# Kernel tuning notes

Hardware: AMD Instinct MI355X
Metric: run time of the kernel (lower is better)

The kernel has to match this reference:

```python
import jax, jax.numpy as jnp
from jax import lax
import numpy as np

B, T, H, W = 32, 16, 64, 64
LAT, HID, NL = 256, 256, 10
CH = 32  # c_hid
DN = ('NCHW', 'OIHW', 'NCHW')


def setup_inputs() -> dict:
    key = jax.random.key(0)
    keys = iter(jax.random.split(key, 64))
    def rn(shape, scale=0.05):
        return jax.random.normal(next(keys), shape, jnp.float32) * scale
    inp = {}
    inp['x'] = jax.random.normal(next(keys), (B, T, H, W), jnp.float32)
    inp['t'] = jax.random.normal(next(keys), (B, T, H, W), jnp.float32)
    # encoder convs (torch Conv2d weight layout: (out,in,kh,kw))
    inp['ec1_w'] = rn((CH, 1, 3, 3));        inp['ec1_b'] = rn((CH,))
    inp['ec2_w'] = rn((CH, CH, 3, 3));       inp['ec2_b'] = rn((CH,))
    inp['ec3_w'] = rn((2*CH, CH, 3, 3));     inp['ec3_b'] = rn((2*CH,))
    inp['ec4_w'] = rn((2*CH, 2*CH, 3, 3));   inp['ec4_b'] = rn((2*CH,))
    inp['ec5_w'] = rn((2*CH, 2*CH, 3, 3));   inp['ec5_b'] = rn((2*CH,))
    inp['el_w'] = rn((LAT, 2*CH*8*8));       inp['el_b'] = rn((LAT,))
    # decoder (ConvTranspose2d weight layout: (in,out,kh,kw))
    inp['dl_w'] = rn((2*CH*8*8, LAT));       inp['dl_b'] = rn((2*CH*8*8,))
    inp['dt1_w'] = rn((2*CH, 2*CH, 3, 3));   inp['dt1_b'] = rn((2*CH,))
    inp['dc1_w'] = rn((2*CH, 2*CH, 3, 3));   inp['dc1_b'] = rn((2*CH,))
    inp['dt2_w'] = rn((2*CH, CH, 3, 3));     inp['dt2_b'] = rn((CH,))
    inp['dc2_w'] = rn((CH, CH, 3, 3));       inp['dc2_b'] = rn((CH,))
    inp['dt3_w'] = rn((CH, 1, 3, 3));        inp['dt3_b'] = rn((1,))
    # 10 stacked LSTMCells (LAT == HID so layer 0 weight shape matches the rest)
    inp['Wih'] = rn((NL, 4*HID, HID))
    inp['Whh'] = rn((NL, 4*HID, HID))
    inp['bih'] = rn((NL, 4*HID))
    inp['bhh'] = rn((NL, 4*HID))
    inp['lw'] = rn((LAT, HID));  inp['lb'] = rn((LAT,))
    return inp


def gelu(v):
    return jax.nn.gelu(v, approximate=False)


def conv(x, w, b, stride):
    y = lax.conv_general_dilated(x, w, (stride, stride), [(1, 1), (1, 1)], dimension_numbers=DN)
    return y + b[None, :, None, None]


def tconv(x, w, b):
    # torch ConvTranspose2d(k=3, stride=2, padding=1, output_padding=1):
    # flip kernel, swap in/out channels, lhs_dilation=2, pad (lo=1, hi=2)
    wf = jnp.transpose(w[:, :, ::-1, ::-1], (1, 0, 2, 3))
    y = lax.conv_general_dilated(x, wf, (1, 1), [(1, 2), (1, 2)], lhs_dilation=(2, 2), dimension_numbers=DN)
    return y + b[None, :, None, None]


def reference(x, t, ec1_w, ec1_b, ec2_w, ec2_b, ec3_w, ec3_b, ec4_w, ec4_b, ec5_w, ec5_b,
              el_w, el_b, dl_w, dl_b, dt1_w, dt1_b, dc1_w, dc1_b, dt2_w, dt2_b,
              dc2_w, dc2_b, dt3_w, dt3_b, Wih, Whh, bih, bhh, lw, lb):

    def encode(imgs):                              # (N,1,64,64) -> (N,LAT)
        h = gelu(conv(imgs, ec1_w, ec1_b, 2))      # 32x32
        h = gelu(conv(h, ec2_w, ec2_b, 1))
        h = gelu(conv(h, ec3_w, ec3_b, 2))         # 16x16
        h = gelu(conv(h, ec4_w, ec4_b, 1))
        h = gelu(conv(h, ec5_w, ec5_b, 2))         # 8x8
        return h.reshape(h.shape[0], -1) @ el_w.T + el_b

    def decode(z):                                 # (N,LAT) -> (N,1,64,64)
        h = gelu(z @ dl_w.T + dl_b).reshape(z.shape[0], 2*CH, 8, 8)
        h = gelu(tconv(h, dt1_w, dt1_b))           # 16x16
        h = gelu(conv(h, dc1_w, dc1_b, 1))
        h = gelu(tconv(h, dt2_w, dt2_b))           # 32x32
        h = gelu(conv(h, dc2_w, dc2_b, 1))
        return jnp.tanh(tconv(h, dt3_w, dt3_b))    # 64x64

    def cell_stack(h, c, xin):                     # h,c: (NL,B,HID)
        hs, cs = [], []
        prev = xin
        for l in range(NL):
            z = prev @ Wih[l].T + bih[l] + h[l] @ Whh[l].T + bhh[l]
            i, f, g, o = jnp.split(z, 4, axis=-1)
            cl = jax.nn.sigmoid(f) * c[l] + jax.nn.sigmoid(i) * jnp.tanh(g)
            hl = jax.nn.sigmoid(o) * jnp.tanh(cl)
            hs.append(hl); cs.append(cl); prev = hl
        out = prev @ lw.T + lb                     # skip=False
        return jnp.stack(hs), jnp.stack(cs), out

    f_x_t = jnp.concatenate((x, t), axis=1)        # (B,2T,H,W)
    z_x_t = encode(f_x_t.reshape(-1, 1, H, W)).reshape(B, 2 * T, LAT)
    z_x = z_x_t[:, :T]

    h0 = jnp.zeros((NL, B, HID), x.dtype)
    c0 = jnp.zeros((NL, B, HID), x.dtype)

    def step1(carry, xin):
        h, c = carry
        h, c, out = cell_stack(h, c, xin)
        return (h, c), out

    (hT, cT), outs1 = lax.scan(step1, (h0, c0), jnp.swapaxes(z_x, 0, 1))

    def step2(carry, _):
        h, c, xin = carry
        h, c, out = cell_stack(h, c, xin)
        return (h, c, out), out

    _, outs2 = lax.scan(step2, (hT, cT, outs1[-1]), None, length=T)

    outputs = jnp.swapaxes(jnp.concatenate((outs1, outs2), axis=0), 0, 1)  # (B,2T,LAT)
    y_t = outputs[:, T - 1:-1]                    # (B,T,LAT)

    f_t_ = decode(y_t.reshape(B * T, LAT))        # (B*T,1,H,W)
    loss_pred = jnp.mean((f_t_ - f_x_t[:, T:].reshape(-1, 1, H, W)) ** 2)

    f_x_ = decode(z_x.reshape(B * T, LAT))        # rec_loss=True branch
    loss_rec = jnp.mean((f_x_ - f_x_t[:, :T].reshape(-1, 1, H, W)) ** 2)

    return loss_pred, loss_rec, f_t_.reshape(B, T, H, W)
```

## Files before the change

### kernel.cpp

```cpp
#include <hip/hip_runtime.h>
#include <math.h>

#define DEV __device__ __forceinline__

typedef __attribute__((ext_vector_type(8))) short bf8_t;
typedef __attribute__((ext_vector_type(4))) float f4_t;
typedef unsigned short us;

DEV float sigm_f(float v) { return 1.0f / (1.0f + __expf(-v)); }
DEV float tanh_f(float v) { return fmaf(-2.0f, 1.0f / (1.0f + __expf(2.0f * v)), 1.0f); }
DEV float gelu_f(float v) {
  float u = 0.79788456080f * fmaf(0.044715f * v * v, v, v);
  return 0.5f * v * (1.0f + tanh_f(u));
}
DEV unsigned short f2bf(float f) {
  unsigned u = __float_as_uint(f);
  u = (u + 0x7FFFu + ((u >> 16) & 1u)) >> 16;
  return (unsigned short)u;
}
DEV void astore(unsigned* p, unsigned v) {
  __hip_atomic_store(p, v, __ATOMIC_RELAXED, __HIP_MEMORY_SCOPE_AGENT);
}

DEV void prep_norm(int li, const float* w, us* wb, int CIN) {
  int ci = li % CIN;
  int r  = li / CIN;
  int kw = r % 3; r /= 3;
  int kh = r % 3;
  int co = r / 3;
  wb[li] = f2bf(w[((co * CIN + ci) * 3 + kh) * 3 + kw]);
}
DEV void prep_par(int li, const float* w, us* wb, int COUT, int CIN) {
  const int TAPORD[9] = {4, 3, 5, 1, 7, 0, 2, 6, 8};
  int ci = li % CIN;
  int r  = li / CIN;
  int ti = r % 9;
  int co = r / 9;
  int tap = TAPORD[ti];
  int kh = tap / 3, kw = tap % 3;
  wb[li] = f2bf(w[((ci * COUT + co) * 3 + (2 - kh)) * 3 + (2 - kw)]);
}

__global__ __launch_bounds__(256) void prepw_all_k(
    const float* __restrict__ ec2, const float* __restrict__ ec3,
    const float* __restrict__ ec4, const float* __restrict__ ec5,
    const float* __restrict__ dt1, const float* __restrict__ dc1,
    const float* __restrict__ dt2, const float* __restrict__ dc2,
    us* __restrict__ o_ec2, us* __restrict__ o_ec3,
    us* __restrict__ o_ec4, us* __restrict__ o_ec5,
    us* __restrict__ o_dt1, us* __restrict__ o_dc1,
    us* __restrict__ o_dt2, us* __restrict__ o_dc2)
{
  int idx = blockIdx.x * 256 + threadIdx.x;
  if (idx < 9216)        prep_norm(idx,          ec2, o_ec2, 32);
  else if (idx < 27648)  prep_norm(idx - 9216,   ec3, o_ec3, 32);
  else if (idx < 64512)  prep_norm(idx - 27648,  ec4, o_ec4, 64);
  else if (idx < 101376) prep_norm(idx - 64512,  ec5, o_ec5, 64);
  else if (idx < 138240) prep_par (idx - 101376, dt1, o_dt1, 64, 64);
  else if (idx < 175104) prep_norm(idx - 138240, dc1, o_dc1, 64);
  else if (idx < 193536) prep_par (idx - 175104, dt2, o_dt2, 32, 64);
  else if (idx < 202752) prep_norm(idx - 193536, dc2, o_dc2, 32);
}

__global__ __launch_bounds__(256) void prep_misc_k(
    const float* __restrict__ Wih, const float* __restrict__ lw,
    const float* __restrict__ lb,  const float* __restrict__ bih,
    us* __restrict__ wih0b, us* __restrict__ lwTb,
    us* __restrict__ lwbp,  float* __restrict__ beff)
{
  int idx = blockIdx.x * 256 + threadIdx.x;
  if (idx < 262144) {
    wih0b[idx] = f2bf(Wih[idx]);
  } else if (idx < 327680) {
    int i = idx - 262144;
    int n = i & 255, kcol = i >> 8;
    lwTb[i] = f2bf(lw[(size_t)n * 256 + kcol]);
  } else if (idx < 393216) {
    int i = idx - 327680;
    lwbp[i] = f2bf(lw[i]);
  } else if (idx < 394240) {
    int j = idx - 393216;
    float s = bih[j];
    const float* row = Wih + (size_t)j * 256;
    for (int n = 0; n < 256; ++n) s = fmaf(row[n], lb[n], s);
    beff[j] = s;
  }
}

__global__ __launch_bounds__(256) void prep_eldl_k(
    const float* __restrict__ el_w, const float* __restrict__ dl_w,
    us* __restrict__ elWb, us* __restrict__ dlWb)
{
  int idx = blockIdx.x * 256 + threadIdx.x;
  if (idx < 1048576) {
    int i = idx;
    int kn = i & 4095, n = i >> 12;
    elWb[i] = f2bf(el_w[(size_t)n * 4096 + ((kn & 63) * 64 + (kn >> 6))]);
  } else {
    int i = idx - 1048576;
    int k = i & 255, nout = i >> 8;
    dlWb[i] = f2bf(dl_w[(size_t)((nout & 63) * 64 + (nout >> 6)) * 256 + k]);
  }
}

__global__ __launch_bounds__(256) void prep_wl1_k(
    const us* __restrict__ src, us* __restrict__ wb)
{
  int idx = blockIdx.x * 256 + threadIdx.x;
  int e = idx & 7, lane = (idx >> 3) & 63, ks = (idx >> 9) & 7, nt = idx >> 12;
  wb[idx] = src[(size_t)(nt * 16 + (lane & 15)) * 256 + ks * 32 + (lane >> 4) * 8 + e];
}

__global__ __launch_bounds__(256) void ec1_k(
    const float* __restrict__ x, const float* __restrict__ t,
    const float* __restrict__ w, const float* __restrict__ bias,
    us* __restrict__ out)
{
  __shared__ float sw[288];
  __shared__ float sb[32];
  for (int i = threadIdx.x; i < 288; i += 256) sw[i] = w[i];
  if (threadIdx.x < 32) sb[threadIdx.x] = bias[threadIdx.x];
  __syncthreads();
  int idx = blockIdx.x * 256 + threadIdx.x;
  int ox = idx & 31, oy = (idx >> 5) & 31, n = idx >> 10;
  int b = n >> 5, j = n & 31;
  const float* ip = (j < 16) ? (x + (size_t)(b * 16 + j) * 4096)
                             : (t + (size_t)(b * 16 + j - 16) * 4096);
  float pv[9];
#pragma unroll
  for (int kh = 0; kh < 3; ++kh) {
    int iy = oy * 2 + kh - 1;
#pragma unroll
    for (int kw = 0; kw < 3; ++kw) {
      int ix = ox * 2 + kw - 1;
      pv[kh * 3 + kw] = ((unsigned)iy < 64u && (unsigned)ix < 64u) ? ip[iy * 64 + ix] : 0.f;
    }
  }
  us u[32];
#pragma unroll
  for (int co = 0; co < 32; ++co) {
    float a = sb[co];
#pragma unroll
    for (int i = 0; i < 9; ++i) a = fmaf(pv[i], sw[co * 9 + i], a);
    u[co] = f2bf(gelu_f(a));
  }
  us* op = out + (size_t)idx * 32;
#pragma unroll
  for (int p = 0; p < 4; ++p) {
    uint4 v;
    v.x = u[p*8+0] | (u[p*8+1] << 16);
    v.y = u[p*8+2] | (u[p*8+3] << 16);
    v.z = u[p*8+4] | (u[p*8+5] << 16);
    v.w = u[p*8+6] | (u[p*8+7] << 16);
    *(uint4*)&op[p * 8] = v;
  }
}

template<int CIN, int COUT, int HIN, int WIN, int TH, int TW, int MODE>
DEV void convmf_tile(const us* __restrict__ in, const us* __restrict__ wb,
                     const float* __restrict__ bias, us* __restrict__ out,
                     int vb, int nofs, us* lds)
{
  constexpr int HO  = (MODE == 1) ? HIN / 2 : HIN;
  constexpr int WO  = (MODE == 1) ? WIN / 2 : WIN;
  constexpr int TIH = (MODE == 1) ? 2 * TH + 1 : TH + 2;
  constexpr int TIW = (MODE == 1) ? 2 * TW + 1 : TW + 2;
  constexpr int TIWP = (TIW & 1) ? TIW : TIW + 1;
  constexpr int CG  = CIN / 8;
  constexpr int K   = 9 * CIN;
  constexpr int KS  = K / 32;
  constexpr int NT  = COUT / 16;
  constexpr int MT  = (TH * TW) / 16;
  constexpr int MPW = MT / 4;
  constexpr int TY  = HO / TH, TX = WO / TW;

  const int n = nofs + vb / (TY * TX);
  const int trem = vb % (TY * TX);
  const int ty0 = (trem / TX) * TH, tx0 = (trem % TX) * TW;

  constexpr int ENT = TIH * TIW * CG;
  for (int e = threadIdx.x; e < ENT; e += 256) {
    int txx = e % TIW;
    int rr  = e / TIW;
    int cg  = rr % CG;
    int tyy = rr / CG;
    int iy, ix; bool ok;
    if (MODE == 0) {
      iy = ty0 + tyy - 1; ix = tx0 + txx - 1;
      ok = (unsigned)iy < (unsigned)HIN && (unsigned)ix < (unsigned)WIN;
    } else {
      iy = 2 * ty0 + tyy - 1; ix = 2 * tx0 + txx - 1;
      ok = (unsigned)iy < (unsigned)HIN && (unsigned)ix < (unsigned)WIN;
    }
    int4 val = {0, 0, 0, 0};
    if (ok) val = *(const int4*)&in[(((size_t)n * HIN + iy) * WIN + ix) * CIN + cg * 8];
    *(int4*)&lds[(size_t)((tyy * CG + cg) * TIWP + txx) * 8] = val;
  }
  __syncthreads();

  const int lane = threadIdx.x & 63, wv = threadIdx.x >> 6;
  const int l15 = lane & 15, l4 = lane >> 4;

  f4_t acc[MPW][NT] = {};
  for (int ks = 0; ks < KS; ++ks) {
    const int tap = (ks * 32) / CIN;
    const int kh = tap / 3, kw = tap % 3;
    const int cb = ((ks * 32) % CIN) / 8 + l4;
    bf8_t bf[NT];
#pragma unroll
    for (int nt = 0; nt < NT; ++nt)
      bf[nt] = *(const bf8_t*)&wb[(size_t)(nt * 16 + l15) * K + ks * 32 + 8 * l4];
#pragma unroll
    for (int mi = 0; mi < MPW; ++mi) {
      int m = (wv * MPW + mi) * 16 + l15;
      int oy = m / TW, ox = m % TW;
      int rt = ((MODE == 1) ? 2 * oy : oy) + kh;
      int ct = ((MODE == 1) ? 2 * ox : ox) + kw;
      bf8_t a = *(const bf8_t*)&lds[(size_t)((rt * CG + cb) * TIWP + ct) * 8];
#pragma unroll
      for (int nt = 0; nt < NT; ++nt)
        acc[mi][nt] = __builtin_amdgcn_mfma_f32_16x16x32_bf16(a, bf[nt], acc[mi][nt], 0, 0, 0);
    }
  }

#pragma unroll
  for (int mi = 0; mi < MPW; ++mi) {
    int mbase = (wv * MPW + mi) * 16;
#pragma unroll
    for (int nt = 0; nt < NT; ++nt) {
      int co = nt * 16 + l15;
      float bv = bias[co];
#pragma unroll
      for (int r = 0; r < 4; ++r) {
        int m = mbase + l4 * 4 + r;
        int oy = m / TW, ox = m % TW;
        float v = acc[mi][nt][r] + bv;
        out[(((size_t)n * HO + ty0 + oy) * WO + (tx0 + ox)) * COUT + co] = f2bf(gelu_f(v));
      }
    }
  }
  __syncthreads();
}

template<int CIN, int COUT, int HIN, int WIN, int TH, int TW, int MODE>
__global__ __launch_bounds__(256) void convmf_k(
    const us* __restrict__ in, const us* __restrict__ wb,
    const float* __restrict__ bias, us* __restrict__ out)
{
  constexpr int TIH = (MODE == 1) ? 2 * TH + 1 : TH + 2;
  constexpr int TIW = (MODE == 1) ? 2 * TW + 1 : TW + 2;
  constexpr int TIWP = (TIW & 1) ? TIW : TIW + 1;
  __shared__ us lds[TIH * TIWP * (CIN / 8) * 8];
  convmf_tile<CIN, COUT, HIN, WIN, TH, TW, MODE>(in, wb, bias, out, blockIdx.x, 0, lds);
}

template<int CIN, int COUT, int HIN, int WIN, int SH, int SW>
DEV void tconvp_tile(const us* __restrict__ in, const us* __restrict__ wbp,
                     const float* __restrict__ bias, us* __restrict__ out,
                     int vb, int nofs, us* lds)
{
  constexpr int HO = 2 * HIN, WO = 2 * WIN;
  constexpr int CG = CIN / 8;
  constexpr int TIH = SH + 1, TIW = SW + 1;
  constexpr int NT = COUT / 16;
  constexpr int MPW_P = (SH * SW) / 16;
  constexpr int TY = HIN / SH, TX = WIN / SW;

  const int n = nofs + vb / (TY * TX);
  const int trem = vb % (TY * TX);
  const int toy = trem / TX, tox = trem % TX;
  const int ty0s = toy * SH, tx0s = tox * SW;

  constexpr int ENT = TIH * TIW * CG;
  for (int e = threadIdx.x; e < ENT; e += 256) {
    int txx = e % TIW;
    int rr  = e / TIW;
    int cg  = rr % CG;
    int tyy = rr / CG;
    int iy = ty0s + tyy, ix = tx0s + txx;
    int4 val = {0, 0, 0, 0};
    if (iy < HIN && ix < WIN)
      val = *(const int4*)&in[(((size_t)n * HIN + iy) * WIN + ix) * CIN + cg * 8];
    *(int4*)&lds[(size_t)((tyy * CG + cg) * TIW + txx) * 8] = val;
  }
  __syncthreads();

  const int lane = threadIdx.x & 63, wv = threadIdx.x >> 6;
  const int l15 = lane & 15, l4 = lane >> 4;
  const int dy = wv >> 1, dx = wv & 1;
  const int NXT = 1 + dx;
  const int KS2 = ((1 + dy) * (1 + dx) * CIN) / 32;
  const int koff = (dy ? (dx ? 5 : 3) : (dx ? 1 : 0)) * CIN;

  f4_t acc[MPW_P][NT] = {};
  for (int ks = 0; ks < KS2; ++ks) {
    const int tapi = (ks * 32) / CIN;
    const int cb = ((ks * 32) % CIN) / 8 + l4;
    const int ra = tapi / NXT, rb = tapi % NXT;
    bf8_t bf[NT];
#pragma unroll
    for (int nt = 0; nt < NT; ++nt)
      bf[nt] = *(const bf8_t*)&wbp[(size_t)(nt * 16 + l15) * 9 * CIN + koff + ks * 32 + 8 * l4];
#pragma unroll
    for (int mi = 0; mi < MPW_P; ++mi) {
      int m = mi * 16 + l15;
      int i = m / SW, j = m % SW;
      bf8_t a = *(const bf8_t*)&lds[(size_t)(((i + ra) * CG + cb) * TIW + (j + rb)) * 8];
#pragma unroll
      for (int nt = 0; nt < NT; ++nt)
        acc[mi][nt] = __builtin_amdgcn_mfma_f32_16x16x32_bf16(a, bf[nt], acc[mi][nt], 0, 0, 0);
    }
  }

#pragma unroll
  for (int mi = 0; mi < MPW_P; ++mi) {
#pragma unroll
    for (int nt = 0; nt < NT; ++nt) {
      int co = nt * 16 + l15;
      float bv = bias[co];
#pragma unroll
      for (int r = 0; r < 4; ++r) {
        int m = mi * 16 + l4 * 4 + r;
        int i = m / SW, j = m % SW;
        int orow = 2 * (ty0s + i) + dy, ocol = 2 * (tx0s + j) + dx;
        float v = acc[mi][nt][r] + bv;
        out[(((size_t)n * HO + orow) * WO + ocol) * COUT + co] = f2bf(gelu_f(v));
      }
    }
  }
  __syncthreads();
}

template<int CIN, int COUT, int HIN, int WIN, int SH, int SW>
__global__ __launch_bounds__(256) void tconvp_k(
    const us* __restrict__ in, const us* __restrict__ wbp,
    const float* __restrict__ bias, us* __restrict__ out)
{
  __shared__ us lds[(SH + 1) * (SW + 1) * (CIN / 8) * 8];
  tconvp_tile<CIN, COUT, HIN, WIN, SH, SW>(in, wbp, bias, out, blockIdx.x, 0, lds);
}

template<int BIASMODE, bool GELU, int OUTMODE>
__global__ __launch_bounds__(256) void gemm16_k(
    const us* __restrict__ A, const us* __restrict__ Bw,
    const float* __restrict__ bias, void* __restrict__ Cv, int M, int N, int K)
{
  const int lane = threadIdx.x & 63, wv = threadIdx.x >> 6;
  const int l15 = lane & 15, l4 = lane >> 4;
  const int mbase = blockIdx.y * 64 + wv * 16;
  const int nbase = blockIdx.x * 64;
  f4_t acc[4] = {};
  for (int k0 = 0; k0 < K; k0 += 32) {
    bf8_t a = *(const bf8_t*)&A[(size_t)(mbase + l15) * K + k0 + 8 * l4];
#pragma unroll
    for (int nt = 0; nt < 4; ++nt) {
      bf8_t b = *(const bf8_t*)&Bw[(size_t)(nbase + nt * 16 + l15) * K + k0 + 8 * l4];
      acc[nt] = __builtin_amdgcn_mfma_f32_16x16x32_bf16(a, b, acc[nt], 0, 0, 0);
    }
  }
#pragma unroll
  for (int nt = 0; nt < 4; ++nt) {
    int col = nbase + nt * 16 + l15;
    float bv = 0.f;
    if (BIASMODE == 0) bv = bias[col];
    if (BIASMODE == 1) bv = bias[(col & 63) * 64 + (col >> 6)];
#pragma unroll
    for (int r = 0; r < 4; ++r) {
      int row = mbase + l4 * 4 + r;
      float v = acc[nt][r] + bv;
      if (GELU) v = gelu_f(v);
      if (OUTMODE == 0)      ((float*)Cv)[(size_t)row * N + col] = v;
      else if (OUTMODE == 1) ((us*)Cv)[(size_t)row * N + col] = f2bf(v);
      else {
        int orow = (row & 31) * 16 + (row >> 5);
        ((us*)Cv)[(size_t)orow * N + col] = f2bf(v);
      }
    }
  }
}

DEV void dlgemm_rec_tile(const us* __restrict__ A, const us* __restrict__ Bw,
                         const float* __restrict__ bias, us* __restrict__ C, int vb)
{
  const int lane = threadIdx.x & 63, wv = threadIdx.x >> 6;
  const int l15 = lane & 15, l4 = lane >> 4;
  const int mbase = 512 + (vb >> 6) * 64 + wv * 16;
  const int nbase = (vb & 63) * 64;
  f4_t acc[4] = {};
  for (int k0 = 0; k0 < 256; k0 += 32) {
    bf8_t a = *(const bf8_t*)&A[(size_t)(mbase + l15) * 256 + k0 + 8 * l4];
#pragma unroll
    for (int nt = 0; nt < 4; ++nt) {
      bf8_t b = *(const bf8_t*)&Bw[(size_t)(nbase + nt * 16 + l15) * 256 + k0 + 8 * l4];
      acc[nt] = __builtin_amdgcn_mfma_f32_16x16x32_bf16(a, b, acc[nt], 0, 0, 0);
    }
  }
#pragma unroll
  for (int nt = 0; nt < 4; ++nt) {
    int col = nbase + nt * 16 + l15;
    float bv = bias[(col & 63) * 64 + (col >> 6)];
#pragma unroll
    for (int r = 0; r < 4; ++r) {
      int row = mbase + l4 * 4 + r;
      C[(size_t)row * 4096 + col] = f2bf(gelu_f(acc[nt][r] + bv));
    }
  }
}

DEV void dt3_rec_tile(const us* __restrict__ in, const float* __restrict__ w,
                      const float* __restrict__ bias, const float* __restrict__ xref,
                      float* __restrict__ partials, int vb, float* sw, float* ws4)
{
  for (int i2 = threadIdx.x; i2 < 288; i2 += 256) sw[i2] = w[i2];
  __syncthreads();
  int idx = vb * 256 + threadIdx.x;
  int j = idx & 31, i = (idx >> 5) & 31, nl = idx >> 10;
  int n = 512 + nl;
  bool okj = (j < 31), oki = (i < 31);
  const us* r00 = in + (((size_t)n * 32 + i) * 32 + j) * 32;
  const us* r01 = r00 + 32;
  const us* r10 = r00 + 1024;
  const us* r11 = r10 + 32;
  float b0 = bias[0];
  float acc00 = b0, acc01 = b0, acc10 = b0, acc11 = b0;
  uint4 z4 = {0, 0, 0, 0};
#pragma unroll
  for (int g2 = 0; g2 < 4; ++g2) {
    uint4 v00 = *(const uint4*)&r00[g2 * 8];
    uint4 v01 = okj ? *(const uint4*)&r01[g2 * 8] : z4;
    uint4 v10 = oki ? *(const uint4*)&r10[g2 * 8] : z4;
    uint4 v11 = (oki && okj) ? *(const uint4*)&r11[g2 * 8] : z4;
    unsigned a00[4] = {v00.x, v00.y, v00.z, v00.w};
    unsigned a01[4] = {v01.x, v01.y, v01.z, v01.w};
    unsigned a10[4] = {v10.x, v10.y, v10.z, v10.w};
    unsigned a11[4] = {v11.x, v11.y, v11.z, v11.w};
#pragma unroll
    for (int h2 = 0; h2 < 4; ++h2) {
      int c0 = (g2 * 8 + h2 * 2) * 9;
      float xl, xh;
      xl = __uint_as_float(a00[h2] << 16); xh = __uint_as_float(a00[h2] & 0xffff0000u);
      acc00 = fmaf(xl, sw[c0 + 4], acc00); acc00 = fmaf(xh, sw[c0 + 13], acc00);
      acc01 = fmaf(xl, sw[c0 + 5], acc01); acc01 = fmaf(xh, sw[c0 + 14], acc01);
      acc10 = fmaf(xl, sw[c0 + 7], acc10); acc10 = fmaf(xh, sw[c0 + 16], acc10);
      acc11 = fmaf(xl, sw[c0 + 8], acc11); acc11 = fmaf(xh, sw[c0 + 17], acc11);
      xl = __uint_as_float(a01[h2] << 16); xh = __uint_as_float(a01[h2] & 0xffff0000u);
      acc01 = fmaf(xl, sw[c0 + 3], acc01); acc01 = fmaf(xh, sw[c0 + 12], acc01);
      acc11 = fmaf(xl, sw[c0 + 6], acc11); acc11 = fmaf(xh, sw[c0 + 15], acc11);
      xl = __uint_as_float(a10[h2] << 16); xh = __uint_as_float(a10[h2] & 0xffff0000u);
      acc10 = fmaf(xl, sw[c0 + 1], acc10); acc10 = fmaf(xh, sw[c0 + 10], acc10);
      acc11 = fmaf(xl, sw[c0 + 2], acc11); acc11 = fmaf(xh, sw[c0 + 11], acc11);
      xl = __uint_as_float(a11[h2] << 16); xh = __uint_as_float(a11[h2] & 0xffff0000u);
      acc11 = fmaf(xl, sw[c0 + 0], acc11); acc11 = fmaf(xh, sw[c0 + 9], acc11);
    }
  }
  float o00 = tanh_f(acc00), o01 = tanh_f(acc01);
  float o10 = tanh_f(acc10), o11 = tanh_f(acc11);
  size_t px = (size_t)(2 * i) * 64 + 2 * j;
  const float* xr = xref + (size_t)nl * 4096;
  float d0 = o00 - xr[px],      d1 = o01 - xr[px + 1];
  float d2 = o10 - xr[px + 64], d3 = o11 - xr[px + 65];
  float s = d0 * d0 + d1 * d1 + d2 * d2 + d3 * d3;
#pragma unroll
  for (int off = 32; off > 0; off >>= 1) s += __shfl_down(s, off);
  if ((threadIdx.x & 63) == 0) ws4[threadIdx.x >> 6] = s;
  __syncthreads();
  if (threadIdx.x == 0) partials[2048 + vb] = ws4[0] + ws4[1] + ws4[2] + ws4[3];
  __syncthreads();
}

__global__ __launch_bounds__(256) void dt3_loss_k(
    const us* __restrict__ in, const float* __restrict__ w,
    const float* __restrict__ bias, const float* __restrict__ tref,
    float* __restrict__ fout, float* __restrict__ partials)
{
  __shared__ float sw[288];
  for (int i2 = threadIdx.x; i2 < 288; i2 += 256) sw[i2] = w[i2];
  __syncthreads();
  int idx = blockIdx.x * 256 + threadIdx.x;
  int j = idx & 31, i = (idx >> 5) & 31, n = idx >> 10;
  bool okj = (j < 31), oki = (i < 31);
  const us* r00 = in + (((size_t)n * 32 + i) * 32 + j) * 32;
  const us* r01 = r00 + 32;
  const us* r10 = r00 + 1024;
  const us* r11 = r10 + 32;
  float b0 = bias[0];
  float acc00 = b0, acc01 = b0, acc10 = b0, acc11 = b0;
  uint4 z4 = {0, 0, 0, 0};
#pragma unroll
  for (int g2 = 0; g2 < 4; ++g2) {
    uint4 v00 = *(const uint4*)&r00[g2 * 8];
    uint4 v01 = okj ? *(const uint4*)&r01[g2 * 8] : z4;
    uint4 v10 = oki ? *(const uint4*)&r10[g2 * 8] : z4;
    uint4 v11 = (oki && okj) ? *(const uint4*)&r11[g2 * 8] : z4;
    unsigned a00[4] = {v00.x, v00.y, v00.z, v00.w};
    unsigned a01[4] = {v01.x, v01.y, v01.z, v01.w};
    unsigned a10[4] = {v10.x, v10.y, v10.z, v10.w};
    unsigned a11[4] = {v11.x, v11.y, v11.z, v11.w};
#pragma unroll
    for (int h2 = 0; h2 < 4; ++h2) {
      int c0 = (g2 * 8 + h2 * 2) * 9;
      float xl, xh;
      xl = __uint_as_float(a00[h2] << 16); xh = __uint_as_float(a00[h2] & 0xffff0000u);
      acc00 = fmaf(xl, sw[c0 + 4], acc00); acc00 = fmaf(xh, sw[c0 + 13], acc00);
      acc01 = fmaf(xl, sw[c0 + 5], acc01); acc01 = fmaf(xh, sw[c0 + 14], acc01);
      acc10 = fmaf(xl, sw[c0 + 7], acc10); acc10 = fmaf(xh, sw[c0 + 16], acc10);
      acc11 = fmaf(xl, sw[c0 + 8], acc11); acc11 = fmaf(xh, sw[c0 + 17], acc11);
      xl = __uint_as_float(a01[h2] << 16); xh = __uint_as_float(a01[h2] & 0xffff0000u);
      acc01 = fmaf(xl, sw[c0 + 3], acc01); acc01 = fmaf(xh, sw[c0 + 12], acc01);
      acc11 = fmaf(xl, sw[c0 + 6], acc11); acc11 = fmaf(xh, sw[c0 + 15], acc11);
      xl = __uint_as_float(a10[h2] << 16); xh = __uint_as_float(a10[h2] & 0xffff0000u);
      acc10 = fmaf(xl, sw[c0 + 1], acc10); acc10 = fmaf(xh, sw[c0 + 10], acc10);
      acc11 = fmaf(xl, sw[c0 + 2], acc11); acc11 = fmaf(xh, sw[c0 + 11], acc11);
      xl = __uint_as_float(a11[h2] << 16); xh = __uint_as_float(a11[h2] & 0xffff0000u);
      acc11 = fmaf(xl, sw[c0 + 0], acc11); acc11 = fmaf(xh, sw[c0 + 9], acc11);
    }
  }
  float o00 = tanh_f(acc00), o01 = tanh_f(acc01);
  float o10 = tanh_f(acc10), o11 = tanh_f(acc11);
  size_t px = (size_t)(2 * i) * 64 + 2 * j;
  float* fb = fout + (size_t)n * 4096;
  fb[px] = o00;      fb[px + 1] = o01;
  fb[px + 64] = o10; fb[px + 65] = o11;
  const float* tr = tref + (size_t)n * 4096;
  float d0 = o00 - tr[px],      d1 = o01 - tr[px + 1];
  float d2 = o10 - tr[px + 64], d3 = o11 - tr[px + 65];
  float s = d0 * d0 + d1 * d1 + d2 * d2 + d3 * d3;
#pragma unroll
  for (int off = 32; off > 0; off >>= 1) s += __shfl_down(s, off);
  __shared__ float ws4[4];
  if ((threadIdx.x & 63) == 0) ws4[threadIdx.x >> 6] = s;
  __syncthreads();
  if (threadIdx.x == 0) partials[blockIdx.x] = ws4[0] + ws4[1] + ws4[2] + ws4[3];
}

__global__ __launch_bounds__(256) void loss_final_k(
    const float* __restrict__ partials, float* __restrict__ out01)
{
  __shared__ float red[256];
  int base = blockIdx.x * 2048;
  float s = 0.f;
  for (int i = threadIdx.x; i < 2048; i += 256) s += partials[base + i];
  red[threadIdx.x] = s;
  __syncthreads();
#pragma unroll
  for (int st = 128; st > 0; st >>= 1) {
    if (threadIdx.x < st) red[threadIdx.x] += red[threadIdx.x + st];
    __syncthreads();
  }
  if (threadIdx.x == 0) out01[blockIdx.x] = red[0] * (1.0f / 2097152.0f);
}

__global__ __launch_bounds__(256) void gather_z_k(
    const float* __restrict__ z, us* __restrict__ ydec)
{
  int idx = blockIdx.x * 256 + threadIdx.x;
  int rr = idx >> 8, k = idx & 255;
  int b = rr >> 4, tt = rr & 15;
  ydec[(size_t)(512 + rr) * 256 + k] = f2bf(z[(size_t)(b * 32 + tt) * 256 + k]);
}

#define LSTM_NB 160

DEV void gridbar(unsigned* bar, unsigned target) {
  __syncthreads();
  if (threadIdx.x == 0) {
    __hip_atomic_fetch_add(bar, 1u, __ATOMIC_RELEASE, __HIP_MEMORY_SCOPE_AGENT);
    unsigned spins = 0;
    while (__hip_atomic_load(bar, __ATOMIC_RELAXED, __HIP_MEMORY_SCOPE_AGENT) < target) {
      __builtin_amdgcn_s_sleep(2);
      if (++spins > (1u << 24)) break;
    }
    (void)__hip_atomic_load(bar, __ATOMIC_ACQUIRE, __HIP_MEMORY_SCOPE_AGENT);
  }
  __syncthreads();
}

DEV void spin_min16s(unsigned* f, unsigned tgt) {
  if ((int)tgt <= 0) return;
  unsigned spins = 0;
  for (;;) {
    unsigned m = 0xffffffffu;
#pragma unroll
    for (int i = 0; i < 16; ++i) {
      unsigned v = __hip_atomic_load(f + i * 32, __ATOMIC_RELAXED, __HIP_MEMORY_SCOPE_AGENT);
      m = v < m ? v : m;
    }
    if (m >= tgt) return;
    if (++spins > (1u << 22)) return;
  }
}

__global__ __launch_bounds__(256, 1) void mega_k(
    const float* __restrict__ z, const float* __restrict__ Wih,
    const float* __restrict__ Whh, const us* __restrict__ meffb,
    const float* __restrict__ bih, const float* __restrict__ bhh,
    const float* __restrict__ beff,
    us* __restrict__ zbf, us* __restrict__ hbf, us* __restrict__ h9sav,
    unsigned* __restrict__ bar,
    const us* __restrict__ ydec, const us* __restrict__ dlWb,
    const float* __restrict__ dl_b,
    const us* __restrict__ wbp_dt1, const float* __restrict__ dt1_b,
    const us* __restrict__ wb_dc1,  const float* __restrict__ dc1_b,
    const us* __restrict__ wbp_dt2, const float* __restrict__ dt2_b,
    const us* __restrict__ wb_dc2,  const float* __restrict__ dc2_b,
    const float* __restrict__ dt3_w, const float* __restrict__ dt3_b,
    const float* __restrict__ xref,
    us* __restrict__ bufA, us* __restrict__ bufB,
    float* __restrict__ partials)
{
  __shared__ __align__(16) unsigned char smem[109568];

  const int tid = threadIdx.x;
  const int bid = blockIdx.x;

  if (bid < 160) {
    us*    s_w   = (us*)smem;
    us*    s_x   = (us*)(smem + 65536);
    us*    s_h   = (us*)(smem + 81920);
    float* zsm   = (float*)(smem + 98304);
    float* cls   = (float*)(smem + 107008);
    float* sbias = (float*)(smem + 109056);
    float* sb2   = (float*)(smem + 109312);

    const int l   = bid >> 4;
    const int jg  = bid & 15;
    const int col0 = jg * 16;
    const int lane = tid & 63, g = tid >> 6;
    const int l15 = lane & 15, l4 = lane >> 4;
    const int gtid = bid * 256 + tid;

    unsigned* fl = bar + 64;
    unsigned* fown = fl + (size_t)l * 16 * 32;

    for (int i = gtid; i < 16 * 32 * 256; i += LSTM_NB * 256) {
      int k = i & 255, r = i >> 8;
      int tt = r >> 5, b = r & 31;
      zbf[i] = f2bf(z[(size_t)(b * 32 + tt) * 256 + k]);
    }
    for (int i = gtid; i < 81920; i += LSTM_NB * 256) hbf[81920 + i] = 0;
    for (int c = tid; c < 4096; c += 256) {
      int gm = c >> 9;
      int gg = gm >> 1, m = gm & 1;
      int c2 = c & 511;
      int ks = c2 >> 6, ln = c2 & 63;
      const float* src = (m == 0 ? Wih : Whh)
          + ((size_t)l * 1024 + gg * 256 + jg * 16 + (ln & 15)) * 256
          + ks * 32 + (ln >> 4) * 8;
      us tmp[8];
#pragma unroll
      for (int e = 0; e < 8; ++e) tmp[e] = f2bf(src[e]);
      *(int4*)&s_w[(size_t)c * 8] = *(int4*)tmp;
    }
    for (int i = tid; i < 512; i += 256) cls[i] = 0.f;
    if (tid < 64) {
      int gg = tid >> 4, j = tid & 15;
      sbias[tid] = bih[l * 1024 + gg * 256 + col0 + j]
                 + bhh[l * 1024 + gg * 256 + col0 + j];
      sb2[tid]   = beff[gg * 256 + col0 + j] + bhh[gg * 256 + col0 + j];
    }

    gridbar(bar, LSTM_NB);

    for (int t = 0; t <= 30; ++t) {
      const int cur = t & 1, prv = cur ^ 1;
      const bool p2 = (t >= 16);
      const bool p2l0 = p2 && (l == 0);

      if (tid == 0) {
        spin_min16s(fown, (unsigned)t);
        (void)__hip_atomic_load(fown, __ATOMIC_ACQUIRE, __HIP_MEMORY_SCOPE_AGENT);
      }
      __syncthreads();
      const us* hb = hbf + (size_t)((prv * 10 + l) * 32) * 256;
#pragma unroll
      for (int i = 0; i < 4; ++i) {
        int c = tid + i * 256;
        int sw = (c & ~31) | ((c & 31) ^ ((c >> 5) & 7));
        *(int4*)&s_h[(size_t)sw * 8] = *(const int4*)&hb[(size_t)c * 8];
      }
      if (tid == 0) {
        if (l == 0) {
          if (t >= 16) spin_min16s(fl + (size_t)9 * 16 * 32, (unsigned)t);
        } else {
          spin_min16s(fl + (size_t)(l - 1) * 16 * 32, (unsigned)(t + 1));
        }
        if (t >= 2) {
          if (l < 9) spin_min16s(fl + (size_t)(l + 1) * 16 * 32, (unsigned)(t - 1));
          else if (t >= 17) spin_min16s(fl, (unsigned)t);
        }
        (void)__hip_atomic_load(fown, __ATOMIC_ACQUIRE, __HIP_MEMORY_SCOPE_AGENT);
      }
      __syncthreads();
      const us* xb =
          (l == 0) ? (p2 ? (hbf + (size_t)((prv * 10 + 9) * 32) * 256)
                         : (zbf + (size_t)t * 32 * 256))
                   : (hbf + (size_t)((cur * 10 + l - 1) * 32) * 256);
#pragma unroll
      for (int i = 0; i < 4; ++i) {
        int c = tid + i * 256;
        int sw = (c & ~31) | ((c & 31) ^ ((c >> 5) & 7));
        *(int4*)&s_x[(size_t)sw * 8] = *(const int4*)&xb[(size_t)c * 8];
      }
      __syncthreads();
      f4_t a0 = {}, a1 = {}, b0 = {}, b1 = {};
#pragma unroll
      for (int ks = 0; ks < 8; ++ks) {
        bf8_t bwi = *(const bf8_t*)&s_w[(size_t)((g * 2 + 0) * 4096 + ks * 512 + lane * 8)];
        bf8_t bwh = *(const bf8_t*)&s_w[(size_t)((g * 2 + 1) * 4096 + ks * 512 + lane * 8)];
        int cx0 = (l15 << 5) | ((ks * 4 + l4) ^ (l15 & 7));
        int cx1 = ((16 + l15) << 5) | ((ks * 4 + l4) ^ (l15 & 7));
        bf8_t ax0 = *(const bf8_t*)&s_x[(size_t)cx0 * 8];
        bf8_t ax1 = *(const bf8_t*)&s_x[(size_t)cx1 * 8];
        bf8_t ah0 = *(const bf8_t*)&s_h[(size_t)cx0 * 8];
        bf8_t ah1 = *(const bf8_t*)&s_h[(size_t)cx1 * 8];
        a0 = __builtin_amdgcn_mfma_f32_16x16x32_bf16(ax0, bwi, a0, 0, 0, 0);
        a1 = __builtin_amdgcn_mfma_f32_16x16x32_bf16(ax1, bwi, a1, 0, 0, 0);
        b0 = __builtin_amdgcn_mfma_f32_16x16x32_bf16(ah0, bwh, b0, 0, 0, 0);
        b1 = __builtin_amdgcn_mfma_f32_16x16x32_bf16(ah1, bwh, b1, 0, 0, 0);
      }
#pragma unroll
      for (int r = 0; r < 4; ++r) {
        zsm[(g * 32 + l4 * 4 + r) * 17 + l15] = a0[r] + b0[r];
        zsm[(g * 32 + 16 + l4 * 4 + r) * 17 + l15] = a1[r] + b1[r];
      }
      __syncthreads();
#pragma unroll
      for (int half = 0; half < 2; ++half) {
        int e = tid + half * 256;
        int b = e >> 4, j = e & 15;
        float zi = zsm[(0 * 32 + b) * 17 + j] + (p2l0 ? sb2[j]      : sbias[j]);
        float zf = zsm[(1 * 32 + b) * 17 + j] + (p2l0 ? sb2[16 + j] : sbias[16 + j]);
        float zg = zsm[(2 * 32 + b) * 17 + j] + (p2l0 ? sb2[32 + j] : sbias[32 + j]);
        float zo = zsm[(3 * 32 + b) * 17 + j] + (p2l0 ? sb2[48 + j] : sbias[48 + j]);
        float cold = cls[b * 16 + j];
        float cn = sigm_f(zf) * cold + sigm_f(zi) * tanh_f(zg);
        cls[b * 16 + j] = cn;
        float hn = sigm_f(zo) * tanh_f(cn);
        float hn_hi = __shfl_down(hn, 1);
        if (!(j & 1)) {
          unsigned pk = (unsigned)f2bf(hn) | ((unsigned)f2bf(hn_hi) << 16);
          astore((unsigned*)&hbf[(size_t)((cur * 10 + l) * 32 + b) * 256 + col0 + j], pk);
          if (l == 9 && t >= 15)
            astore((unsigned*)&h9sav[(size_t)((t - 15) * 32 + b) * 256 + col0 + j], pk);
        }
      }
      __syncthreads();
      if (tid == 0)
        __hip_atomic_store(&fown[jg * 32], (unsigned)(t + 1),
                           __ATOMIC_RELEASE, __HIP_MEMORY_SCOPE_AGENT);
      if (l == 0 && t == 15) {
        for (int c = tid; c < 2048; c += 256) {
          int gg = c >> 9, c2 = c & 511;
          const us* src = meffb + ((size_t)(gg * 16 + jg) * 8) * 512;
          *(int4*)&s_w[(size_t)((gg * 2) * 512 + c2) * 8] = *(const int4*)&src[(size_t)c2 * 8];
        }
        __syncthreads();
      }
    }
  } else {
    us* lds = (us*)smem;
    float* swq = (float*)(smem + 49152);
    float* ws4 = (float*)(smem + 50432);
    unsigned* bar96 = bar + 32;
    const int wg = bid - 160;
    int ep2 = 0;

    for (int vb = wg; vb < 512; vb += 96)
      dlgemm_rec_tile(ydec, dlWb, dl_b, bufB, vb);
    ++ep2; gridbar(bar96, (unsigned)(ep2 * 96));
    for (int vb = wg; vb < 512; vb += 96)
      tconvp_tile<64, 64, 8, 8, 8, 8>(bufB, wbp_dt1, dt1_b, bufA, vb, 512, lds);
    ++ep2; gridbar(bar96, (unsigned)(ep2 * 96));
    for (int vb = wg; vb < 512; vb += 96)
      convmf_tile<64, 64, 16, 16, 16, 16, 0>(bufA, wb_dc1, dc1_b, bufB, vb, 512, lds);
    ++ep2; gridbar(bar96, (unsigned)(ep2 * 96));
    for (int vb = wg; vb < 1024; vb += 96)
      tconvp_tile<64, 32, 16, 16, 8, 16>(bufB, wbp_dt2, dt2_b, bufA, vb, 512, lds);
    ++ep2; gridbar(bar96, (unsigned)(ep2 * 96));
    for (int vb = wg; vb < 2048; vb += 96)
      convmf_tile<32, 32, 32, 32, 16, 16, 0>(bufA, wb_dc2, dc2_b, bufB, vb, 512, lds);
    ++ep2; gridbar(bar96, (unsigned)(ep2 * 96));
    for (int vb = wg; vb < 2048; vb += 96)
      dt3_rec_tile(bufB, dt3_w, dt3_b, xref, partials, vb, swq, ws4);
  }
}

extern "C" void kernel_launch(void* const* d_in, const int* in_sizes, int n_in,
                              void* d_out, int out_size, void* d_ws, size_t ws_size,
                              hipStream_t stream) {
  const float* x     = (const float*)d_in[0];
  const float* t     = (const float*)d_in[1];
  const float* ec1_w = (const float*)d_in[2];
  const float* ec1_b = (const float*)d_in[3];
  const float* ec2_w = (const float*)d_in[4];
  const float* ec2_b = (const float*)d_in[5];
  const float* ec3_w = (const float*)d_in[6];
  const float* ec3_b = (const float*)d_in[7];
  const float* ec4_w = (const float*)d_in[8];
  const float* ec4_b = (const float*)d_in[9];
  const float* ec5_w = (const float*)d_in[10];
  const float* ec5_b = (const float*)d_in[11];
  const float* el_w  = (const float*)d_in[12];
  const float* el_b  = (const float*)d_in[13];
  const float* dl_w  = (const float*)d_in[14];
  const float* dl_b  = (const float*)d_in[15];
  const float* dt1_w = (const float*)d_in[16];
  const float* dt1_b = (const float*)d_in[17];
  const float* dc1_w = (const float*)d_in[18];
  const float* dc1_b = (const float*)d_in[19];
  const float* dt2_w = (const float*)d_in[20];
  const float* dt2_b = (const float*)d_in[21];
  const float* dc2_w = (const float*)d_in[22];
  const float* dc2_b = (const float*)d_in[23];
  const float* dt3_w = (const float*)d_in[24];
  const float* dt3_b = (const float*)d_in[25];
  const float* Wih   = (const float*)d_in[26];
  const float* Whh   = (const float*)d_in[27];
  const float* bih   = (const float*)d_in[28];
  const float* bhh   = (const float*)d_in[29];
  const float* lw    = (const float*)d_in[30];
  const float* lb    = (const float*)d_in[31];
  float* out = (float*)d_out;

  char* base = (char*)d_ws;
  size_t off = 0;
  auto alloc = [&](size_t bytes) -> char* {
    char* p = base + off;
    off += (bytes + 255) & ~(size_t)255;
    return p;
  };
  unsigned* bar   = (unsigned*)alloc(32768);
  float* zbuf     = (float*)alloc((size_t)1024 * 256 * 4);
  us*    zbf      = (us*)alloc((size_t)16 * 32 * 256 * 2);
  us*    hbf      = (us*)alloc((size_t)2 * 10 * 32 * 256 * 2);
  us*    h9sav    = (us*)alloc((size_t)16 * 32 * 256 * 2);
  us*    ydec     = (us*)alloc((size_t)1024 * 256 * 2);
  float* partials = (float*)alloc((size_t)16384 * 4);
  us* wb_ec2 = (us*)alloc((size_t)32 * 288 * 2);
  us* wb_ec3 = (us*)alloc((size_t)64 * 288 * 2);
  us* wb_ec4 = (us*)alloc((size_t)64 * 576 * 2);
  us* wb_ec5 = (us*)alloc((size_t)64 * 576 * 2);
  us* wbp_dt1 = (us*)alloc((size_t)64 * 576 * 2);
  us* wb_dc1 = (us*)alloc((size_t)64 * 576 * 2);
  us* wbp_dt2 = (us*)alloc((size_t)32 * 576 * 2);
  us* wb_dc2 = (us*)alloc((size_t)32 * 288 * 2);
  us* elWb   = (us*)alloc((size_t)256 * 4096 * 2);
  us* dlWb   = (us*)alloc((size_t)4096 * 256 * 2);
  us* wih0b  = (us*)alloc((size_t)1024 * 256 * 2);
  us* lwTb   = (us*)alloc((size_t)256 * 256 * 2);
  us* lwbp   = (us*)alloc((size_t)256 * 256 * 2);
  us* meffp  = (us*)alloc((size_t)1024 * 256 * 2);
  us* meffb  = (us*)alloc((size_t)1024 * 256 * 2);
  float* beff = (float*)alloc((size_t)1024 * 4);
  us* enc5   = (us*)alloc((size_t)1024 * 4096 * 2);
  us* bufA   = (us*)alloc((size_t)1024 * 32 * 32 * 32 * 2);
  us* bufB   = (us*)alloc((size_t)1024 * 32 * 32 * 32 * 2);
  (void)in_sizes; (void)n_in; (void)out_size; (void)ws_size;

  hipMemsetAsync(bar, 0, 32768, stream);

  prepw_all_k<<<792, 256, 0, stream>>>(ec2_w, ec3_w, ec4_w, ec5_w,
                                       dt1_w, dc1_w, dt2_w, dc2_w,
                                       wb_ec2, wb_ec3, wb_ec4, wb_ec5,
                                       wbp_dt1, wb_dc1, wbp_dt2, wb_dc2);
  prep_misc_k<<<1540, 256, 0, stream>>>(Wih, lw, lb, bih, wih0b, lwTb, lwbp, beff);
  prep_eldl_k<<<8192, 256, 0, stream>>>(el_w, dl_w, elWb, dlWb);
  gemm16_k<2, false, 1><<<dim3(4, 16), 256, 0, stream>>>(wih0b, lwTb, lb, meffp, 1024, 256, 256);
  prep_wl1_k<<<1024, 256, 0, stream>>>(meffp, meffb);

  ec1_k<<<4096, 256, 0, stream>>>(x, t, ec1_w, ec1_b, bufA);
  convmf_k<32, 32, 32, 32, 16, 16, 0><<<4096, 256, 0, stream>>>(bufA, wb_ec2, ec2_b, bufB);
  convmf_k<32, 64, 32, 32, 16, 16, 1><<<1024, 256, 0, stream>>>(bufB, wb_ec3, ec3_b, bufA);
  convmf_k<64, 64, 16, 16, 16, 16, 0><<<1024, 256, 0, stream>>>(bufA, wb_ec4, ec4_b, bufB);
  convmf_k<64, 64, 16, 16, 8, 8, 1><<<1024, 256, 0, stream>>>(bufB, wb_ec5, ec5_b, enc5);
  gemm16_k<0, false, 0><<<dim3(4, 16), 256, 0, stream>>>(enc5, elWb, el_b, zbuf, 1024, 256, 4096);

  gather_z_k<<<512, 256, 0, stream>>>(zbuf, ydec);

  mega_k<<<256, 256, 0, stream>>>(zbuf, Wih, Whh, meffb, bih, bhh, beff,
                                  zbf, hbf, h9sav, bar,
                                  ydec, dlWb, dl_b,
                                  wbp_dt1, dt1_b, wb_dc1, dc1_b,
                                  wbp_dt2, dt2_b, wb_dc2, dc2_b,
                                  dt3_w, dt3_b, x, bufA, bufB, partials);

  gemm16_k<0, false, 2><<<dim3(4, 8), 256, 0, stream>>>(
      h9sav, lwbp, lb, ydec, 512, 256, 256);
  gemm16_k<1, true, 1><<<dim3(64, 8), 256, 0, stream>>>(ydec, dlWb, dl_b, bufB, 1024, 4096, 256);
  tconvp_k<64, 64, 8, 8, 8, 8><<<512, 256, 0, stream>>>(bufB, wbp_dt1, dt1_b, bufA);
  convmf_k<64, 64, 16, 16, 16, 16, 0><<<512, 256, 0, stream>>>(bufA, wb_dc1, dc1_b, bufB);
  tconvp_k<64, 32, 16, 16, 8, 16><<<1024, 256, 0, stream>>>(bufB, wbp_dt2, dt2_b, bufA);
  convmf_k<32, 32, 32, 32, 16, 16, 0><<<2048, 256, 0, stream>>>(bufA, wb_dc2, dc2_b, bufB);
  dt3_loss_k<<<2048, 256, 0, stream>>>(bufB, dt3_w, dt3_b, t, out + 2, partials);
  loss_final_k<<<2, 256, 0, stream>>>(partials, out);
}
```

Baseline: 1.247 ms.

## Encode only x frames, split-K the encoder linear, fuse prep kernels

The encoder now runs only on the x frames, because the latents of the t frames are never used. This halves the conv encoder grids and the size of the encoder output buffer. The encoder linear layer becomes a split-K MFMA GEMM with a combine kernel that writes the bf16 latents straight into the LSTM input and decoder buffers, removing the gather kernel and the conversion loop inside the mega kernel. The three weight-prep kernels are merged into one launch. The split-K path adds an fp32 partial buffer and an extra reduction pass.

```diff
diff --git a/kernel.cpp b/kernel.cpp
--- a/kernel.cpp
+++ b/kernel.cpp
@@ -41,7 +41,7 @@
   wb[li] = f2bf(w[((ci * COUT + co) * 3 + (2 - kh)) * 3 + (2 - kw)]);
 }
 
-__global__ __launch_bounds__(256) void prepw_all_k(
+__global__ __launch_bounds__(256) void prep_all_k(
     const float* __restrict__ ec2, const float* __restrict__ ec3,
     const float* __restrict__ ec4, const float* __restrict__ ec5,
     const float* __restrict__ dt1, const float* __restrict__ dc1,
@@ -49,57 +49,52 @@
     us* __restrict__ o_ec2, us* __restrict__ o_ec3,
     us* __restrict__ o_ec4, us* __restrict__ o_ec5,
     us* __restrict__ o_dt1, us* __restrict__ o_dc1,
-    us* __restrict__ o_dt2, us* __restrict__ o_dc2)
-{
-  int idx = blockIdx.x * 256 + threadIdx.x;
-  if (idx < 9216)        prep_norm(idx,          ec2, o_ec2, 32);
-  else if (idx < 27648)  prep_norm(idx - 9216,   ec3, o_ec3, 32);
-  else if (idx < 64512)  prep_norm(idx - 27648,  ec4, o_ec4, 64);
-  else if (idx < 101376) prep_norm(idx - 64512,  ec5, o_ec5, 64);
-  else if (idx < 138240) prep_par (idx - 101376, dt1, o_dt1, 64, 64);
-  else if (idx < 175104) prep_norm(idx - 138240, dc1, o_dc1, 64);
-  else if (idx < 193536) prep_par (idx - 175104, dt2, o_dt2, 32, 64);
-  else if (idx < 202752) prep_norm(idx - 193536, dc2, o_dc2, 32);
-}
-
-__global__ __launch_bounds__(256) void prep_misc_k(
+    us* __restrict__ o_dt2, us* __restrict__ o_dc2,
     const float* __restrict__ Wih, const float* __restrict__ lw,
     const float* __restrict__ lb,  const float* __restrict__ bih,
     us* __restrict__ wih0b, us* __restrict__ lwTb,
-    us* __restrict__ lwbp,  float* __restrict__ beff)
-{
-  int idx = blockIdx.x * 256 + threadIdx.x;
-  if (idx < 262144) {
-    wih0b[idx] = f2bf(Wih[idx]);
-  } else if (idx < 327680) {
-    int i = idx - 262144;
-    int n = i & 255, kcol = i >> 8;
-    lwTb[i] = f2bf(lw[(size_t)n * 256 + kcol]);
-  } else if (idx < 393216) {
-    int i = idx - 327680;
-    lwbp[i] = f2bf(lw[i]);
-  } else if (idx < 394240) {
-    int j = idx - 393216;
-    float s = bih[j];
-    const float* row = Wih + (size_t)j * 256;
-    for (int n = 0; n < 256; ++n) s = fmaf(row[n], lb[n], s);
-    beff[j] = s;
-  }
-}
-
-__global__ __launch_bounds__(256) void prep_eldl_k(
+    us* __restrict__ lwbp,  float* __restrict__ beff,
     const float* __restrict__ el_w, const float* __restrict__ dl_w,
     us* __restrict__ elWb, us* __restrict__ dlWb)
 {
   int idx = blockIdx.x * 256 + threadIdx.x;
-  if (idx < 1048576) {
-    int i = idx;
-    int kn = i & 4095, n = i >> 12;
-    elWb[i] = f2bf(el_w[(size_t)n * 4096 + ((kn & 63) * 64 + (kn >> 6))]);
+  if (idx < 202752) {
+    if (idx < 9216)        prep_norm(idx,          ec2, o_ec2, 32);
+    else if (idx < 27648)  prep_norm(idx - 9216,   ec3, o_ec3, 32);
+    else if (idx < 64512)  prep_norm(idx - 27648,  ec4, o_ec4, 64);
+    else if (idx < 101376) prep_norm(idx - 64512,  ec5, o_ec5, 64);
+    else if (idx < 138240) prep_par (idx - 101376, dt1, o_dt1, 64, 64);
+    else if (idx < 175104) prep_norm(idx - 138240, dc1, o_dc1, 64);
+    else if (idx < 193536) prep_par (idx - 175104, dt2, o_dt2, 32, 64);
+    else                   prep_norm(idx - 193536, dc2, o_dc2, 32);
+  } else if (idx < 596992) {
+    int i2 = idx - 202752;
+    if (i2 < 262144) {
+      wih0b[i2] = f2bf(Wih[i2]);
+    } else if (i2 < 327680) {
+      int i = i2 - 262144;
+      int n = i & 255, kcol = i >> 8;
+      lwTb[i] = f2bf(lw[(size_t)n * 256 + kcol]);
+    } else if (i2 < 393216) {
+      int i = i2 - 327680;
+      lwbp[i] = f2bf(lw[i]);
+    } else if (i2 < 394240) {
+      int j = i2 - 393216;
+      float s = bih[j];
+      const float* row = Wih + (size_t)j * 256;
+      for (int n = 0; n < 256; ++n) s = fmaf(row[n], lb[n], s);
+      beff[j] = s;
+    }
   } else {
-    int i = idx - 1048576;
-    int k = i & 255, nout = i >> 8;
-    dlWb[i] = f2bf(dl_w[(size_t)((nout & 63) * 64 + (nout >> 6)) * 256 + k]);
+    int i3 = idx - 596992;
+    if (i3 < 1048576) {
+      int kn = i3 & 4095, n = i3 >> 12;
+      elWb[i3] = f2bf(el_w[(size_t)n * 4096 + ((kn & 63) * 64 + (kn >> 6))]);
+    } else {
+      int i = i3 - 1048576;
+      int k = i & 255, nout = i >> 8;
+      dlWb[i] = f2bf(dl_w[(size_t)((nout & 63) * 64 + (nout >> 6)) * 256 + k]);
+    }
   }
 }
 
@@ -112,7 +107,7 @@
 }
 
 __global__ __launch_bounds__(256) void ec1_k(
-    const float* __restrict__ x, const float* __restrict__ t,
+    const float* __restrict__ x,
     const float* __restrict__ w, const float* __restrict__ bias,
     us* __restrict__ out)
 {
@@ -123,9 +118,7 @@
   __syncthreads();
   int idx = blockIdx.x * 256 + threadIdx.x;
   int ox = idx & 31, oy = (idx >> 5) & 31, n = idx >> 10;
-  int b = n >> 5, j = n & 31;
-  const float* ip = (j < 16) ? (x + (size_t)(b * 16 + j) * 4096)
-                             : (t + (size_t)(b * 16 + j - 16) * 4096);
+  const float* ip = x + (size_t)n * 4096;
   float pv[9];
 #pragma unroll
   for (int kh = 0; kh < 3; ++kh) {
@@ -377,6 +370,51 @@
       }
     }
   }
+}
+
+__global__ __launch_bounds__(256) void elgemm_splitk_k(
+    const us* __restrict__ A, const us* __restrict__ Bw,
+    float* __restrict__ zpart)
+{
+  const int lane = threadIdx.x & 63, wv = threadIdx.x >> 6;
+  const int l15 = lane & 15, l4 = lane >> 4;
+  const int mbase = blockIdx.y * 64 + wv * 16;
+  const int nbase = blockIdx.x * 64;
+  const int kbase = blockIdx.z * 512;
+  f4_t acc[4] = {};
+  for (int k0 = kbase; k0 < kbase + 512; k0 += 32) {
+    bf8_t a = *(const bf8_t*)&A[(size_t)(mbase + l15) * 4096 + k0 + 8 * l4];
+#pragma unroll
+    for (int nt = 0; nt < 4; ++nt) {
+      bf8_t b = *(const bf8_t*)&Bw[(size_t)(nbase + nt * 16 + l15) * 4096 + k0 + 8 * l4];
+      acc[nt] = __builtin_amdgcn_mfma_f32_16x16x32_bf16(a, b, acc[nt], 0, 0, 0);
+    }
+  }
+  float* zp = zpart + (size_t)blockIdx.z * 131072;
+#pragma unroll
+  for (int nt = 0; nt < 4; ++nt) {
+    int col = nbase + nt * 16 + l15;
+#pragma unroll
+    for (int r = 0; r < 4; ++r) {
+      int row = mbase + l4 * 4 + r;
+      zp[(size_t)row * 256 + col] = acc[nt][r];
+    }
+  }
+}
+
+__global__ __launch_bounds__(256) void zcombine_k(
+    const float* __restrict__ zpart, const float* __restrict__ el_b,
+    us* __restrict__ zbf, us* __restrict__ ydec)
+{
+  int idx = blockIdx.x * 256 + threadIdx.x;
+  int row = idx >> 8, col = idx & 255;
+  float s = el_b[col];
+#pragma unroll
+  for (int kc = 0; kc < 8; ++kc) s += zpart[(size_t)kc * 131072 + idx];
+  int b = row >> 4, tt = row & 15;
+  us v = f2bf(s);
+  zbf[(size_t)(tt * 32 + b) * 256 + col] = v;
+  ydec[(size_t)(512 + row) * 256 + col] = v;
 }
 
 DEV void dlgemm_rec_tile(const us* __restrict__ A, const us* __restrict__ Bw,
@@ -550,15 +588,6 @@
   if (threadIdx.x == 0) out01[blockIdx.x] = red[0] * (1.0f / 2097152.0f);
 }
 
-__global__ __launch_bounds__(256) void gather_z_k(
-    const float* __restrict__ z, us* __restrict__ ydec)
-{
-  int idx = blockIdx.x * 256 + threadIdx.x;
-  int rr = idx >> 8, k = idx & 255;
-  int b = rr >> 4, tt = rr & 15;
-  ydec[(size_t)(512 + rr) * 256 + k] = f2bf(z[(size_t)(b * 32 + tt) * 256 + k]);
-}
-
 #define LSTM_NB 160
 
 DEV void gridbar(unsigned* bar, unsigned target) {
@@ -591,11 +620,11 @@
 }
 
 __global__ __launch_bounds__(256, 1) void mega_k(
-    const float* __restrict__ z, const float* __restrict__ Wih,
+    const float* __restrict__ Wih,
     const float* __restrict__ Whh, const us* __restrict__ meffb,
     const float* __restrict__ bih, const float* __restrict__ bhh,
     const float* __restrict__ beff,
-    us* __restrict__ zbf, us* __restrict__ hbf, us* __restrict__ h9sav,
+    const us* __restrict__ zbf, us* __restrict__ hbf, us* __restrict__ h9sav,
     unsigned* __restrict__ bar,
     const us* __restrict__ ydec, const us* __restrict__ dlWb,
     const float* __restrict__ dl_b,
@@ -632,11 +661,6 @@
     unsigned* fl = bar + 64;
     unsigned* fown = fl + (size_t)l * 16 * 32;
 
-    for (int i = gtid; i < 16 * 32 * 256; i += LSTM_NB * 256) {
-      int k = i & 255, r = i >> 8;
-      int tt = r >> 5, b = r & 31;
-      zbf[i] = f2bf(z[(size_t)(b * 32 + tt) * 256 + k]);
-    }
     for (int i = gtid; i < 81920; i += LSTM_NB * 256) hbf[81920 + i] = 0;
     for (int c = tid; c < 4096; c += 256) {
       int gm = c >> 9;
@@ -830,7 +854,7 @@
     return p;
   };
   unsigned* bar   = (unsigned*)alloc(32768);
-  float* zbuf     = (float*)alloc((size_t)1024 * 256 * 4);
+  float* zpart    = (float*)alloc((size_t)8 * 512 * 256 * 4);
   us*    zbf      = (us*)alloc((size_t)16 * 32 * 256 * 2);
   us*    hbf      = (us*)alloc((size_t)2 * 10 * 32 * 256 * 2);
   us*    h9sav    = (us*)alloc((size_t)16 * 32 * 256 * 2);
@@ -852,32 +876,31 @@
   us* meffp  = (us*)alloc((size_t)1024 * 256 * 2);
   us* meffb  = (us*)alloc((size_t)1024 * 256 * 2);
   float* beff = (float*)alloc((size_t)1024 * 4);
-  us* enc5   = (us*)alloc((size_t)1024 * 4096 * 2);
+  us* enc5   = (us*)alloc((size_t)512 * 4096 * 2);
   us* bufA   = (us*)alloc((size_t)1024 * 32 * 32 * 32 * 2);
   us* bufB   = (us*)alloc((size_t)1024 * 32 * 32 * 32 * 2);
   (void)in_sizes; (void)n_in; (void)out_size; (void)ws_size;
 
   hipMemsetAsync(bar, 0, 32768, stream);
 
-  prepw_all_k<<<792, 256, 0, stream>>>(ec2_w, ec3_w, ec4_w, ec5_w,
-                                       dt1_w, dc1_w, dt2_w, dc2_w,
-                                       wb_ec2, wb_ec3, wb_ec4, wb_ec5,
-                                       wbp_dt1, wb_dc1, wbp_dt2, wb_dc2);
-  prep_misc_k<<<1540, 256, 0, stream>>>(Wih, lw, lb, bih, wih0b, lwTb, lwbp, beff);
-  prep_eldl_k<<<8192, 256, 0, stream>>>(el_w, dl_w, elWb, dlWb);
+  prep_all_k<<<10524, 256, 0, stream>>>(ec2_w, ec3_w, ec4_w, ec5_w,
+                                        dt1_w, dc1_w, dt2_w, dc2_w,
+                                        wb_ec2, wb_ec3, wb_ec4, wb_ec5,
+                                        wbp_dt1, wb_dc1, wbp_dt2, wb_dc2,
+                                        Wih, lw, lb, bih, wih0b, lwTb, lwbp, beff,
+                                        el_w, dl_w, elWb, dlWb);
   gemm16_k<2, false, 1><<<dim3(4, 16), 256, 0, stream>>>(wih0b, lwTb, lb, meffp, 1024, 256, 256);
   prep_wl1_k<<<1024, 256, 0, stream>>>(meffp, meffb);
 
-  ec1_k<<<4096, 256, 0, stream>>>(x, t, ec1_w, ec1_b, bufA);
-  convmf_k<32, 32, 32, 32, 16, 16, 0><<<4096, 256, 0, stream>>>(bufA, wb_ec2, ec2_b, bufB);
-  convmf_k<32, 64, 32, 32, 16, 16, 1><<<1024, 256, 0, stream>>>(bufB, wb_ec3, ec3_b, bufA);
-  convmf_k<64, 64, 16, 16, 16, 16, 0><<<1024, 256, 0, stream>>>(bufA, wb_ec4, ec4_b, bufB);
-  convmf_k<64, 64, 16, 16, 8, 8, 1><<<1024, 256, 0, stream>>>(bufB, wb_ec5, ec5_b, enc5);
-  gemm16_k<0, false, 0><<<dim3(4, 16), 256, 0, stream>>>(enc5, elWb, el_b, zbuf, 1024, 256, 4096);
-
-  gather_z_k<<<512, 256, 0, stream>>>(zbuf, ydec);
-
-  mega_k<<<256, 256, 0, stream>>>(zbuf, Wih, Whh, meffb, bih, bhh, beff,
+  ec1_k<<<2048, 256, 0, stream>>>(x, ec1_w, ec1_b, bufA);
+  convmf_k<32, 32, 32, 32, 16, 16, 0><<<2048, 256, 0, stream>>>(bufA, wb_ec2, ec2_b, bufB);
+  convmf_k<32, 64, 32, 32, 16, 16, 1><<<512, 256, 0, stream>>>(bufB, wb_ec3, ec3_b, bufA);
+  convmf_k<64, 64, 16, 16, 16, 16, 0><<<512, 256, 0, stream>>>(bufA, wb_ec4, ec4_b, bufB);
+  convmf_k<64, 64, 16, 16, 8, 8, 1><<<512, 256, 0, stream>>>(bufB, wb_ec5, ec5_b, enc5);
+  elgemm_splitk_k<<<dim3(4, 8, 8), 256, 0, stream>>>(enc5, elWb, zpart);
+  zcombine_k<<<512, 256, 0, stream>>>(zpart, el_b, zbf, ydec);
+
+  mega_k<<<256, 256, 0, stream>>>(Wih, Whh, meffb, bih, bhh, beff,
                                   zbf, hbf, h9sav, bar,
                                   ydec, dlWb, dl_b,
                                   wbp_dt1, dt1_b, wb_dc1, dc1_b,
```

Result: faster. 1.048 ms (-15.9%).
